# Performance work log

Hardware: AMD Instinct MI355X
Metric: run time of the kernel (lower is better)

## Reference

```python
import jax, jax.numpy as jnp
import numpy as np

N_HEADS = 4
HEAD_DIM = 64
NEG_SLOPE = 0.2
TIME_PE_DIM = 16


def time_pe(date):
    # TimePositionalEncoding: sin/cos features; 8 sin + 8 cos == pe_dim (16), no projection needed
    t = date.astype(jnp.float32) / 10000.0
    div = jnp.exp(jnp.arange(0, TIME_PE_DIM, 2, dtype=jnp.float32) * (-jnp.log(10000.0) / TIME_PE_DIM))
    arg = t[:, None] * div[None, :]  # [N, 8]
    return jnp.concatenate([jnp.sin(arg), jnp.cos(arg)], axis=-1)  # [N, 16]


def pearl_pe(x, edge_index, Wp, bp):
    # PEARL positional embedding approximated as mean-neighbor aggregation over the
    # union of all relations followed by a learned linear + tanh -> [N, 32]
    N = x.shape[0]
    src = edge_index[:, 0, :].reshape(-1)
    dst = edge_index[:, 1, :].reshape(-1)
    agg = jax.ops.segment_sum(x[src], dst, num_segments=N)
    deg = jax.ops.segment_sum(jnp.ones_like(dst, jnp.float32), dst, num_segments=N)
    agg = agg / jnp.maximum(deg, 1.0)[:, None]
    return jnp.tanh(agg @ Wp + bp)


def gatv2(x, src, dst, Wl, Wr, att, b):
    # GATv2 message passing for one edge type; dropout is identity (eval mode)
    N = x.shape[0]
    xl = (x @ Wl).reshape(N, N_HEADS, HEAD_DIM)
    xr = (x @ Wr).reshape(N, N_HEADS, HEAD_DIM)
    m = xl[src] + xr[dst]                                   # [E, H, C]
    e = jnp.sum(jax.nn.leaky_relu(m, NEG_SLOPE) * att, -1)  # [E, H]
    emax = jax.ops.segment_max(e, dst, num_segments=N)
    emax = jnp.where(jnp.isfinite(emax), emax, 0.0)
    ex = jnp.exp(e - emax[dst])
    denom = jax.ops.segment_sum(ex, dst, num_segments=N)
    alpha = ex / (denom[dst] + 1e-16)                       # segment softmax over in-edges
    out = jax.ops.segment_sum(xl[src] * alpha[..., None], dst, num_segments=N)
    return out.reshape(N, N_HEADS * HEAD_DIM) + b


def rel_agg(h_rel, W, b, a):
    # attention-weighted combination across relation outputs: h_rel [N, R, hidden]
    s = jnp.einsum('nrh,h->nr', jnp.tanh(h_rel @ W + b), a)
    w = jax.nn.softmax(s, axis=-1)
    return jnp.einsum('nr,nrh->nh', w, h_rel)


def gnn_layer(h, edge_index, Wl, Wr, att, b, aW, ab, aa):
    R = edge_index.shape[0]
    # HeteroConv aggr='sum': sum GATv2 outputs across the 5 relations
    conv_sum = gatv2(h, edge_index[0, 0], edge_index[0, 1], Wl[0], Wr[0], att[0], b[0])
    for r in range(1, R):
        conv_sum = conv_sum + gatv2(h, edge_index[r, 0], edge_index[r, 1], Wl[r], Wr[r], att[r], b[r])
    # original forward feeds conv_output['stock'] for every relation key (identical copies)
    h_rel = jnp.broadcast_to(conv_sum[:, None, :], (conv_sum.shape[0], R, conv_sum.shape[1]))
    h = rel_agg(h_rel, aW, ab, aa)
    return jax.nn.relu(h)  # dropout identity in eval


def reference(x, date_tensor, edge_index, pearl_W, pearl_b, Wl0, Wr0, att0, b0,
              Wl1, Wr1, att1, b1, aggW, aggb, agga, out_W1, out_b1, out_W2, out_b2):
    pe = pearl_pe(x, edge_index, pearl_W, pearl_b)          # [N, 32]
    tpe = time_pe(date_tensor)                              # [N, 16]
    h = jnp.concatenate([x, pe, tpe], axis=1)               # [N, 112]
    h = gnn_layer(h, edge_index, Wl0, Wr0, att0, b0, aggW[0], aggb[0], agga[0])
    h = gnn_layer(h, edge_index, Wl1, Wr1, att1, b1, aggW[1], aggb[1], agga[1])
    h = jax.nn.relu(h @ out_W1 + out_b1)
    return h @ out_W2 + out_b2                              # [N, 3]


def setup_inputs():
    key = jax.random.key(0)
    ks = jax.random.split(key, 20)
    N, E, R = 20000, 320000, 5
    IN, PE, HID = 64, 32, 256
    IN0 = IN + PE + TIME_PE_DIM  # 112

    def nrm(k, shp, sc=0.05):
        return jax.random.normal(k, shp, jnp.float32) * sc

    return {
        'x': jax.random.normal(ks[0], (N, IN), jnp.float32),
        'date_tensor': jax.random.randint(ks[1], (N,), 0, 20000, jnp.int32),
        'edge_index': jax.random.randint(ks[2], (R, 2, E), 0, N, jnp.int32),
        'pearl_W': nrm(ks[3], (IN, PE)),
        'pearl_b': jnp.zeros((PE,), jnp.float32),
        'Wl0': nrm(ks[4], (R, IN0, HID)),
        'Wr0': nrm(ks[5], (R, IN0, HID)),
        'att0': nrm(ks[6], (R, N_HEADS, HEAD_DIM)),
        'b0': jnp.zeros((R, HID), jnp.float32),
        'Wl1': nrm(ks[7], (R, HID, HID)),
        'Wr1': nrm(ks[8], (R, HID, HID)),
        'att1': nrm(ks[9], (R, N_HEADS, HEAD_DIM)),
        'b1': jnp.zeros((R, HID), jnp.float32),
        'aggW': nrm(ks[10], (2, HID, HID)),
        'aggb': jnp.zeros((2, HID), jnp.float32),
        'agga': nrm(ks[11], (2, HID)),
        'out_W1': nrm(ks[12], (HID, HID // 2)),
        'out_b1': jnp.zeros((HID // 2,), jnp.float32),
        'out_W2': nrm(ks[13], (HID // 2, 3)),
        'out_b2': jnp.zeros((3,), jnp.float32),
    }
```

## Files before the change

### kernel.cpp

```cpp
#include <hip/hip_runtime.h>
#include <math.h>

typedef __bf16 bf16x8 __attribute__((ext_vector_type(8)));
typedef __bf16 bf16x4 __attribute__((ext_vector_type(4)));
typedef float f32x4 __attribute__((ext_vector_type(4)));
typedef unsigned short u16x8 __attribute__((ext_vector_type(8)));

#define GLD16(src, dst)                                                        \
    __builtin_amdgcn_global_load_lds(                                          \
        (const __attribute__((address_space(1))) void*)(src),                  \
        (__attribute__((address_space(3))) void*)(dst), 16, 0, 0)

__device__ inline float bf2f(unsigned short u) {
    union { unsigned int i; float f; } c;
    c.i = ((unsigned int)u) << 16;
    return c.f;
}


__global__ __launch_bounds__(256) void count_kernel(const int* __restrict__ ei,
                                                    int* __restrict__ cnt, int N, int E) {
    int idx = blockIdx.x * 256 + threadIdx.x;
    if (idx >= 5 * E) return;
    int r = idx / E;
    int e = idx - r * E;
    int dst = ei[(size_t)r * 2 * E + E + e];
    atomicAdd(&cnt[r * N + dst], 1);
}

__global__ __launch_bounds__(256) void scanA_kernel(const int* __restrict__ cnt,
                                                    int* __restrict__ off,
                                                    int* __restrict__ csums, int N, int NC) {
    int r = blockIdx.y, c = blockIdx.x, t = threadIdx.x;
    int idx0 = c * 1024 + t * 4;
    int v0 = (idx0 + 0 < N) ? cnt[r * N + idx0 + 0] : 0;
    int v1 = (idx0 + 1 < N) ? cnt[r * N + idx0 + 1] : 0;
    int v2 = (idx0 + 2 < N) ? cnt[r * N + idx0 + 2] : 0;
    int v3 = (idx0 + 3 < N) ? cnt[r * N + idx0 + 3] : 0;
    int ts = v0 + v1 + v2 + v3;
    __shared__ int sd[256];
    sd[t] = ts;
    __syncthreads();
    for (int s = 1; s < 256; s <<= 1) {
        int add = (t >= s) ? sd[t - s] : 0;
        __syncthreads();
        sd[t] += add;
        __syncthreads();
    }
    int excl = sd[t] - ts;
    size_t base = (size_t)r * (N + 1);
    if (idx0 + 0 < N) off[base + idx0 + 0] = excl;
    if (idx0 + 1 < N) off[base + idx0 + 1] = excl + v0;
    if (idx0 + 2 < N) off[base + idx0 + 2] = excl + v0 + v1;
    if (idx0 + 3 < N) off[base + idx0 + 3] = excl + v0 + v1 + v2;
    if (t == 255) csums[r * NC + c] = sd[255];
}

__global__ __launch_bounds__(64) void scanB_kernel(int* __restrict__ csums,
                                                   int* __restrict__ off, int N, int NC) {
    int r = threadIdx.x;
    if (r < 5) {
        int run = 0;
        for (int c = 0; c < NC; c++) {
            int t = csums[r * NC + c];
            csums[r * NC + c] = run;
            run += t;
        }
        off[(size_t)r * (N + 1) + N] = run;
    }
}

__global__ __launch_bounds__(256) void scanC_kernel(int* __restrict__ off,
                                                    const int* __restrict__ csums,
                                                    int* __restrict__ cur,
                                                    int N, int NC) {
    int r = blockIdx.y, c = blockIdx.x, t = threadIdx.x;
    int add = csums[r * NC + c];
    int idx0 = c * 1024 + t * 4;
    size_t base = (size_t)r * (N + 1);
#pragma unroll
    for (int j = 0; j < 4; j++)
        if (idx0 + j < N) {
            int v = off[base + idx0 + j] + add;
            off[base + idx0 + j] = v;
            cur[r * N + idx0 + j] = v;
        }
}

__global__ __launch_bounds__(256) void scatter_kernel(const int* __restrict__ ei,
                                                      int* __restrict__ cur,
                                                      unsigned short* __restrict__ srcs,
                                                      int N, int E) {
    int idx = blockIdx.x * 256 + threadIdx.x;
    if (idx >= 5 * E) return;
    int r = idx / E;
    int e = idx - r * E;
    int src = ei[(size_t)r * 2 * E + e];
    int dst = ei[(size_t)r * 2 * E + E + e];
    int pos = atomicAdd(&cur[r * N + dst], 1);
    srcs[(size_t)r * E + pos] = (unsigned short)src;
}


__global__ __launch_bounds__(256) void xcvt_kernel(const float* __restrict__ x,
                                                   unsigned short* __restrict__ xb, int total) {
    int idx = (blockIdx.x * 256 + threadIdx.x) * 4;
    if (idx >= total) return;
    float4 v = *(const float4*)(x + idx);
    __bf16 b0 = (__bf16)v.x, b1 = (__bf16)v.y, b2 = (__bf16)v.z, b3 = (__bf16)v.w;
    unsigned short* p = xb + idx;
    p[0] = *(unsigned short*)&b0;
    p[1] = *(unsigned short*)&b1;
    p[2] = *(unsigned short*)&b2;
    p[3] = *(unsigned short*)&b3;
}


__global__ __launch_bounds__(256) void pearl_h0_kernel(
    const float* __restrict__ x, const unsigned short* __restrict__ xb,
    const int* __restrict__ date,
    const int* __restrict__ off, const unsigned short* __restrict__ srcs,
    const float* __restrict__ pW, const float* __restrict__ pb,
    float* __restrict__ h0, int N, int E) {
    int lane = threadIdx.x & 63;
    int wid = blockIdx.x * 4 + (threadIdx.x >> 6);
    if (wid >= N) return;
    int n = __builtin_amdgcn_readfirstlane(wid);
    int pr = lane >> 5;
    int c2 = (lane & 31) * 2;

    float a0 = 0.f, a1 = 0.f;
    int deg = 0;
    for (int r = 0; r < 5; r++) {
        int kb = off[(size_t)r * (N + 1) + n];
        int ke = off[(size_t)r * (N + 1) + n + 1];
        deg += ke - kb;
        const unsigned short* sp = srcs + (size_t)r * E;
        int k = kb;
        for (; k + 16 <= ke; k += 16) {
            unsigned int u[8];
#pragma unroll
            for (int j = 0; j < 8; j++) {
                int row = sp[k + 2 * j + pr];
                u[j] = *(const unsigned int*)(xb + (size_t)row * 64 + c2);
            }
#pragma unroll
            for (int j = 0; j < 8; j++) {
                a0 += bf2f((unsigned short)(u[j] & 0xffff));
                a1 += bf2f((unsigned short)(u[j] >> 16));
            }
        }
        for (; k + 2 <= ke; k += 2) {
            int row = sp[k + pr];
            unsigned int u = *(const unsigned int*)(xb + (size_t)row * 64 + c2);
            a0 += bf2f((unsigned short)(u & 0xffff));
            a1 += bf2f((unsigned short)(u >> 16));
        }
        if (k < ke) {
            int row = sp[k];
            unsigned int u = *(const unsigned int*)(xb + (size_t)row * 64 + c2);
            if (pr == 0) {
                a0 += bf2f((unsigned short)(u & 0xffff));
                a1 += bf2f((unsigned short)(u >> 16));
            }
        }
    }
    a0 += __shfl_xor(a0, 32, 64);
    a1 += __shfl_xor(a1, 32, 64);
    float dn = fmaxf((float)deg, 1.0f);
    float an0 = a0 / dn, an1 = a1 / dn;

    float s = (lane < 32) ? pb[lane] : 0.f;
#pragma unroll
    for (int cc = 0; cc < 64; cc++) {
        float av = __shfl((cc & 1) ? an1 : an0, cc >> 1, 64);
        if (lane < 32) s = fmaf(av, pW[cc * 32 + lane], s);
    }

    h0[(size_t)n * 112 + lane] = x[(size_t)n * 64 + lane];
    if (lane < 32) h0[(size_t)n * 112 + 64 + lane] = tanhf(s);
    if (lane < 16) {
        float t = (float)date[n] / 10000.0f;
        int i = lane & 7;
        float dv = expf((float)(2 * i) * (-0.57564627324851148f));
        float arg = t * dv;
        h0[(size_t)n * 112 + 96 + lane] = (lane < 8) ? sinf(arg) : cosf(arg);
    }
}


__global__ __launch_bounds__(256) void pack_a_kernel(
    const float* __restrict__ A, __bf16* __restrict__ Ah, __bf16* __restrict__ Al,
    int M, int K, int Mp, int KT) {
    int KG = KT * 4;
    int idx = blockIdx.x * 256 + threadIdx.x;
    if (idx >= Mp * KG) return;
    int m = idx / KG, kgg = idx - m * KG;
    int kt = kgg >> 2, kg = kgg & 3;
    int k0 = kt * 32 + kg * 8;
    int mt = m >> 4, mr = m & 15;
    size_t out = (((size_t)mt * KT + kt) * 64 + kg * 16 + mr) * 8;
    bf16x8 hv, lv;
#pragma unroll
    for (int j = 0; j < 8; j++) {
        int k = k0 + j;
        float v = (m < M && k < K) ? A[(size_t)m * K + k] : 0.f;
        __bf16 h = (__bf16)v;
        hv[j] = h;
        lv[j] = (__bf16)(v - (float)h);
    }
    *(bf16x8*)(Ah + out) = hv;
    *(bf16x8*)(Al + out) = lv;
}


__global__ __launch_bounds__(256) void pack_w_kernel(
    const float* __restrict__ Wl0, const float* __restrict__ Wr0,
    const float* __restrict__ Wl1, const float* __restrict__ Wr1,
    const float* __restrict__ W1,
    __bf16* __restrict__ Wph, __bf16* __restrict__ Wpl) {
    const int S0 = 32768, S1 = 65536;
    int t = blockIdx.y;
    const float* W;
    int K, Nc, KT;
    size_t dst;
    if (t < 5)       { W = Wl0 + (size_t)t * 112 * 256;        K = 112; Nc = 256; KT = 4; dst = (size_t)t * S0; }
    else if (t < 10) { W = Wr0 + (size_t)(t - 5) * 112 * 256;  K = 112; Nc = 256; KT = 4; dst = 163840 + (size_t)(t - 5) * S0; }
    else if (t < 15) { W = Wl1 + (size_t)(t - 10) * 256 * 256; K = 256; Nc = 256; KT = 8; dst = 327680 + (size_t)(t - 10) * S1; }
    else if (t < 20) { W = Wr1 + (size_t)(t - 15) * 256 * 256; K = 256; Nc = 256; KT = 8; dst = 655360 + (size_t)(t - 15) * S1; }
    else             { W = W1;                                  K = 256; Nc = 128; KT = 8; dst = 983040; }
    int entries = (Nc / 16) * KT * 64;
    int idx = blockIdx.x * 256 + threadIdx.x;
    if (idx >= entries) return;
    int nt = idx / (KT * 64);
    int rem = idx - nt * (KT * 64);
    int kt = rem >> 6, lane = rem & 63;
    int kg = lane >> 4, nr = lane & 15;
    bf16x8 hv, lv;
#pragma unroll
    for (int j = 0; j < 8; j++) {
        int k = kt * 32 + kg * 8 + j;
        float v = (k < K) ? W[(size_t)k * Nc + nt * 16 + nr] : 0.f;
        __bf16 h = (__bf16)v;
        hv[j] = h;
        lv[j] = (__bf16)(v - (float)h);
    }
    *(bf16x8*)(Wph + dst + (size_t)idx * 8) = hv;
    *(bf16x8*)(Wpl + dst + (size_t)idx * 8) = lv;
}


__global__ __launch_bounds__(256) void gemm_mfma(
    const __bf16* __restrict__ Ah, const __bf16* __restrict__ Al,
    const __bf16* __restrict__ WLh, const __bf16* __restrict__ WLl,
    const __bf16* __restrict__ WRh, const __bf16* __restrict__ WRl,
    size_t strideB, void* __restrict__ Cl, void* __restrict__ Cr, size_t CstrideBytes,
    int M, int Nout, int KT, const float* __restrict__ bias, int do_relu,
    int npL, int npR, int out_bf16, int NYT, int MTp, int NPANEL) {
    int p = blockIdx.x;
    int stride = 8 * NPANEL;
    int g = p / stride, rem = p % stride;
    int slot = rem % 8, panel = rem / 8;
    int bx = g * 8 + slot;
    if (bx >= MTp) return;
    int by = panel % NYT;
    int side = (panel / NYT) & 1;
    int r = panel / (NYT * 2);

    const __bf16* Bh = (side ? WRh : WLh) + (size_t)r * strideB;
    const __bf16* Bl = (side ? WRl : WLl) + (size_t)r * strideB;
    char* C = (char*)(side ? Cr : Cl) + (size_t)r * CstrideBytes;
    int np = side ? npR : npL;

    __shared__ __bf16 sAh[8 * 512], sAl[8 * 512], sBh[8 * 512], sBl[8 * 512];

    int tid = threadIdx.x, lane = tid & 63, w = tid >> 6;
    int wr = w >> 1, wc = w & 1;

    f32x4 acc[4][4] = {};

    for (int kt = 0; kt < KT; ++kt) {
        int tl = w * 2;
        size_t a0 = ((size_t)(bx * 8 + tl) * KT + kt) * 512 + lane * 8;
        size_t a1 = ((size_t)(bx * 8 + tl + 1) * KT + kt) * 512 + lane * 8;
        size_t b0 = ((size_t)(by * 8 + tl) * KT + kt) * 512 + lane * 8;
        size_t b1 = ((size_t)(by * 8 + tl + 1) * KT + kt) * 512 + lane * 8;
        GLD16(Ah + a0, sAh + tl * 512);
        GLD16(Ah + a1, sAh + (tl + 1) * 512);
        GLD16(Bh + b0, sBh + tl * 512);
        GLD16(Bh + b1, sBh + (tl + 1) * 512);
        if (np >= 2) {
            GLD16(Al + a0, sAl + tl * 512);
            GLD16(Al + a1, sAl + (tl + 1) * 512);
        }
        if (np == 3) {
            GLD16(Bl + b0, sBl + tl * 512);
            GLD16(Bl + b1, sBl + (tl + 1) * 512);
        }
        __syncthreads();

        bf16x8 ah[4], al[4], bh[4], bl[4];
#pragma unroll
        for (int i = 0; i < 4; i++) {
            ah[i] = *(const bf16x8*)(sAh + (wr * 4 + i) * 512 + lane * 8);
            bh[i] = *(const bf16x8*)(sBh + (wc * 4 + i) * 512 + lane * 8);
        }
        if (np >= 2) {
#pragma unroll
            for (int i = 0; i < 4; i++)
                al[i] = *(const bf16x8*)(sAl + (wr * 4 + i) * 512 + lane * 8);
        }
        if (np == 3) {
#pragma unroll
            for (int i = 0; i < 4; i++)
                bl[i] = *(const bf16x8*)(sBl + (wc * 4 + i) * 512 + lane * 8);
        }
#pragma unroll
        for (int i = 0; i < 4; i++)
#pragma unroll
            for (int j = 0; j < 4; j++) {
                acc[i][j] = __builtin_amdgcn_mfma_f32_16x16x32_bf16(ah[i], bh[j], acc[i][j], 0, 0, 0);
                if (np >= 2)
                    acc[i][j] = __builtin_amdgcn_mfma_f32_16x16x32_bf16(al[i], bh[j], acc[i][j], 0, 0, 0);
                if (np == 3)
                    acc[i][j] = __builtin_amdgcn_mfma_f32_16x16x32_bf16(ah[i], bl[j], acc[i][j], 0, 0, 0);
            }
        __syncthreads();
    }

    int rb = bx * 128 + wr * 64, cb = by * 128 + wc * 64;
#pragma unroll
    for (int i = 0; i < 4; i++) {
#pragma unroll
        for (int j = 0; j < 4; j++) {
            int row0 = rb + i * 16 + (lane >> 4) * 4;
            int col = cb + j * 16 + (lane & 15);
            float bv = bias ? bias[col] : 0.f;
#pragma unroll
            for (int q = 0; q < 4; q++) {
                int row = row0 + q;
                if (row < M) {
                    float v = acc[i][j][q] + bv;
                    if (do_relu) v = fmaxf(v, 0.f);
                    if (out_bf16)
                        ((__bf16*)C)[(size_t)row * Nout + col] = (__bf16)v;
                    else
                        ((float*)C)[(size_t)row * Nout + col] = v;
                }
            }
        }
    }
}


__global__ __launch_bounds__(256) void gat5_kernel(
    const unsigned short* __restrict__ xl5, const unsigned short* __restrict__ xr5,
    const float* __restrict__ att,
    const int* __restrict__ csrOff,
    const unsigned short* __restrict__ csrSrc,
    __bf16* __restrict__ Ah, __bf16* __restrict__ Al,
    const float* __restrict__ bvec,
    int N, int E) {
    int lane = threadIdx.x & 63;
    int wid = blockIdx.x * 4 + (threadIdx.x >> 6);
    if (wid >= N) return;
    int n = __builtin_amdgcn_readfirstlane(wid);
    int e = lane >> 4;
    int sub = lane & 15;
    int cb = (sub >> 2) * 64 + (sub & 3) * 16;
    int wc = cb + e * 4;

    float4 cv = {0.f, 0.f, 0.f, 0.f};
#pragma unroll
    for (int r = 0; r < 5; r++) {
        float4 b = *(const float4*)(bvec + r * 256 + wc);
        cv.x += b.x; cv.y += b.y; cv.z += b.z; cv.w += b.w;
    }

    for (int r = 0; r < 5; r++) {
        const unsigned short* xl = xl5 + (size_t)r * N * 256;
        float rv[16], av[16];
        {
            const unsigned short* xrp = xr5 + ((size_t)r * N + n) * 256 + cb;
            u16x8 q0 = *(const u16x8*)(xrp);
            u16x8 q1 = *(const u16x8*)(xrp + 8);
#pragma unroll
            for (int j = 0; j < 8; j++) { rv[j] = bf2f(q0[j]); rv[8 + j] = bf2f(q1[j]); }
#pragma unroll
            for (int j = 0; j < 16; j += 4) {
                float4 a = *(const float4*)(att + r * 256 + cb + j);
                av[j] = a.x; av[j + 1] = a.y; av[j + 2] = a.z; av[j + 3] = a.w;
            }
        }

        float m = -3.0e38f, d = 0.f;
        float A[16];
#pragma unroll
        for (int j = 0; j < 16; j++) A[j] = 0.f;

        const int* off = csrOff + (size_t)r * (N + 1);
        const unsigned short* sp = csrSrc + (size_t)r * E;
        int kb = off[n], ke = off[n + 1];
        if (kb < ke) {
            int kl = ke - 1;
            int ki = kb + e;
            int s = sp[(ki <= kl) ? ki : kl];
            float c[16];
            {
                const unsigned short* xp = xl + (size_t)s * 256 + cb;
                u16x8 q0 = *(const u16x8*)(xp);
                u16x8 q1 = *(const u16x8*)(xp + 8);
#pragma unroll
                for (int j = 0; j < 8; j++) { c[j] = bf2f(q0[j]); c[8 + j] = bf2f(q1[j]); }
            }
            for (int k = kb; k < ke; k += 4) {
                int kn = k + 4 + e;
                int sn = sp[(kn <= kl) ? kn : kl];
                const unsigned short* np_ = xl + (size_t)sn * 256 + cb;
                u16x8 n0 = *(const u16x8*)(np_);
                u16x8 n1 = *(const u16x8*)(np_ + 8);

                float p = 0.f;
#pragma unroll
                for (int j = 0; j < 16; j++) {
                    float t = c[j] + rv[j];
                    t = (t > 0.f) ? t : 0.2f * t;
                    p = fmaf(t, av[j], p);
                }
                p += __shfl_xor(p, 1, 64);
                p += __shfl_xor(p, 2, 64);
                bool valid = (k + e) < ke;
                if (!valid) p = -3.0e38f;

                if (__any(p > m)) {
                    float nm = fmaxf(m, p);
                    float sc = __expf(m - nm);
                    d *= sc;
#pragma unroll
                    for (int j = 0; j < 16; j++) A[j] *= sc;
                    m = nm;
                }
                float wg = valid ? __expf(p - m) : 0.f;
                d += wg;
#pragma unroll
                for (int j = 0; j < 16; j++) A[j] = fmaf(wg, c[j], A[j]);

#pragma unroll
                for (int j = 0; j < 8; j++) { c[j] = bf2f(n0[j]); c[8 + j] = bf2f(n1[j]); }
            }
        }

        float M = fmaxf(m, __shfl_xor(m, 16, 64));
        M = fmaxf(M, __shfl_xor(M, 32, 64));
        float sc = __expf(m - M);
        d *= sc;
        d += __shfl_xor(d, 16, 64);
        d += __shfl_xor(d, 32, 64);
#pragma unroll
        for (int j = 0; j < 16; j++) {
            A[j] *= sc;
            A[j] += __shfl_xor(A[j], 16, 64);
            A[j] += __shfl_xor(A[j], 32, 64);
        }

        float inv = 1.0f / (d + 1e-16f);
        cv.x = fmaf(A[e * 4 + 0], inv, cv.x);
        cv.y = fmaf(A[e * 4 + 1], inv, cv.y);
        cv.z = fmaf(A[e * 4 + 2], inv, cv.z);
        cv.w = fmaf(A[e * 4 + 3], inv, cv.w);
    }

    cv.x = fmaxf(cv.x, 0.f);
    cv.y = fmaxf(cv.y, 0.f);
    cv.z = fmaxf(cv.z, 0.f);
    cv.w = fmaxf(cv.w, 0.f);
    float vv[4] = {cv.x, cv.y, cv.z, cv.w};
    bf16x4 hv, lv;
#pragma unroll
    for (int j = 0; j < 4; j++) {
        __bf16 h = (__bf16)vv[j];
        hv[j] = h;
        lv[j] = (__bf16)(vv[j] - (float)h);
    }
    size_t outp = (((size_t)(n >> 4) * 8 + (wc >> 5)) * 64 + ((wc >> 3) & 3) * 16 + (n & 15)) * 8 + (wc & 7);
    *(bf16x4*)(Ah + outp) = hv;
    *(bf16x4*)(Al + outp) = lv;
}


__global__ __launch_bounds__(256) void head_kernel(const float* __restrict__ hm,
                                                   const float* __restrict__ W2,
                                                   const float* __restrict__ b2,
                                                   float* __restrict__ out, int N) {
    int lane = threadIdx.x & 63;
    int wid = blockIdx.x * 4 + (threadIdx.x >> 6);
    if (wid >= N) return;
    int n = __builtin_amdgcn_readfirstlane(wid);
    float a0 = hm[(size_t)n * 128 + lane];
    float a1 = hm[(size_t)n * 128 + 64 + lane];
    float s0 = a0 * W2[lane * 3 + 0] + a1 * W2[(64 + lane) * 3 + 0];
    float s1 = a0 * W2[lane * 3 + 1] + a1 * W2[(64 + lane) * 3 + 1];
    float s2 = a0 * W2[lane * 3 + 2] + a1 * W2[(64 + lane) * 3 + 2];
#pragma unroll
    for (int sft = 1; sft < 64; sft <<= 1) {
        s0 += __shfl_xor(s0, sft, 64);
        s1 += __shfl_xor(s1, sft, 64);
        s2 += __shfl_xor(s2, sft, 64);
    }
    if (lane == 0) {
        out[(size_t)n * 3 + 0] = s0 + b2[0];
        out[(size_t)n * 3 + 1] = s1 + b2[1];
        out[(size_t)n * 3 + 2] = s2 + b2[2];
    }
}


extern "C" void kernel_launch(void* const* d_in, const int* in_sizes, int n_in,
                              void* d_out, int out_size, void* d_ws, size_t ws_size,
                              hipStream_t stream) {
    const float* x    = (const float*)d_in[0];
    const int* date   = (const int*)d_in[1];
    const int* ei     = (const int*)d_in[2];
    const float* pW   = (const float*)d_in[3];
    const float* pb   = (const float*)d_in[4];
    const float* Wl0  = (const float*)d_in[5];
    const float* Wr0  = (const float*)d_in[6];
    const float* att0 = (const float*)d_in[7];
    const float* b0   = (const float*)d_in[8];
    const float* Wl1  = (const float*)d_in[9];
    const float* Wr1  = (const float*)d_in[10];
    const float* att1 = (const float*)d_in[11];
    const float* b1   = (const float*)d_in[12];
    const float* outW1 = (const float*)d_in[16];
    const float* outb1 = (const float*)d_in[17];
    const float* outW2 = (const float*)d_in[18];
    const float* outb2 = (const float*)d_in[19];
    float* out = (float*)d_out;

    int N = in_sizes[0] / 64;
    int E = in_sizes[2] / 10;
    int Mp = ((N + 127) / 128) * 128;
    int MT = Mp / 128;
    int MT8 = (MT + 7) / 8;
    int NC = (N + 1023) / 1024;

    char* ws = (char*)d_ws;
    size_t o = 0;
    auto alloc = [&](size_t bytes) -> char* {
        char* p = ws + o;
        o += (bytes + 255) & ~(size_t)255;
        return p;
    };
    int* cur               = (int*)alloc((size_t)5 * N * 4);
    int* csrOff            = (int*)alloc((size_t)5 * (N + 1) * 4);
    unsigned short* csrSrc = (unsigned short*)alloc((size_t)5 * E * 2);
    int* csums             = (int*)alloc((size_t)5 * NC * 4);
    unsigned short* xb16   = (unsigned short*)alloc((size_t)N * 64 * 2);
    float* h0              = (float*)alloc((size_t)N * 112 * 4);
    unsigned short* xl5    = (unsigned short*)alloc((size_t)5 * N * 256 * 2);
    unsigned short* xr5    = (unsigned short*)alloc((size_t)5 * N * 256 * 2);
    __bf16* Aph            = (__bf16*)alloc((size_t)Mp * 256 * 2);
    __bf16* Apl            = (__bf16*)alloc((size_t)Mp * 256 * 2);
    __bf16* Wph            = (__bf16*)alloc((size_t)1015808 * 2);
    __bf16* Wpl            = (__bf16*)alloc((size_t)1015808 * 2);
    float* hmid            = (float*)xl5;
    (void)ws_size;

    const size_t S0 = 32768, S1 = 65536;
    const size_t oWl0 = 0, oWr0 = 163840, oWl1 = 327680, oWr1 = 655360, oW1 = 983040;
    size_t xstride = (size_t)N * 256 * 2;

    int totE = 5 * E;

    hipMemsetAsync(cur, 0, (size_t)5 * N * 4, stream);
    count_kernel<<<(totE + 255) / 256, 256, 0, stream>>>(ei, cur, N, E);
    scanA_kernel<<<dim3(NC, 5), 256, 0, stream>>>(cur, csrOff, csums, N, NC);
    scanB_kernel<<<1, 64, 0, stream>>>(csums, csrOff, N, NC);
    scanC_kernel<<<dim3(NC, 5), 256, 0, stream>>>(csrOff, csums, cur, N, NC);
    scatter_kernel<<<(totE + 255) / 256, 256, 0, stream>>>(ei, cur, csrSrc, N, E);

    xcvt_kernel<<<(N * 64 / 4 + 255) / 256, 256, 0, stream>>>(x, xb16, N * 64);
    pearl_h0_kernel<<<(N + 3) / 4, 256, 0, stream>>>(x, xb16, date, csrOff, csrSrc, pW, pb, h0, N, E);

    pack_w_kernel<<<dim3(32, 21, 1), 256, 0, stream>>>(Wl0, Wr0, Wl1, Wr1, outW1, Wph, Wpl);

    pack_a_kernel<<<(Mp * 16 + 255) / 256, 256, 0, stream>>>(h0, Aph, Apl, N, 112, Mp, 4);
    gemm_mfma<<<MT8 * 8 * 20, 256, 0, stream>>>(
        Aph, Apl, Wph + oWl0, Wpl + oWl0, Wph + oWr0, Wpl + oWr0, S0,
        xl5, xr5, xstride, N, 256, 4, nullptr, 0, 1, 1, 1, 2, MT, 20);
    gat5_kernel<<<(N + 3) / 4, 256, 0, stream>>>(xl5, xr5, att0, csrOff, csrSrc,
                                                 Aph, Apl, b0, N, E);

    gemm_mfma<<<MT8 * 8 * 20, 256, 0, stream>>>(
        Aph, Apl, Wph + oWl1, Wpl + oWl1, Wph + oWr1, Wpl + oWr1, S1,
        xl5, xr5, xstride, N, 256, 8, nullptr, 0, 1, 1, 1, 2, MT, 20);
    gat5_kernel<<<(N + 3) / 4, 256, 0, stream>>>(xl5, xr5, att1, csrOff, csrSrc,
                                                 Aph, Apl, b1, N, E);

    gemm_mfma<<<MT8 * 8, 256, 0, stream>>>(
        Aph, Apl, Wph + oW1, Wpl + oW1, Wph + oW1, Wpl + oW1, 0,
        hmid, hmid, 0, N, 128, 8, outb1, 1, 3, 3, 0, 1, MT, 1);
    head_kernel<<<(N + 3) / 4, 256, 0, stream>>>(hmid, outW2, outb2, out, N);
}
```

Measured before the change: 749.9 us.

## Skip unused low-part bf16 writes and load two K-tiles per GEMM barrier

The low-order bf16 split of the activations and weights is now written only where a GEMM actually reads it: the final layer's input and the output-projection weights. The layer GEMMs, which run with one precision pass, no longer produce dead stores. The GEMM also moves to dynamic shared memory and, in the layer GEMMs, loads two K-tiles per synchronisation, which halves the barrier count and issues more loads in flight. The cost is a larger LDS footprint per block (32 KB), which could lower occupancy.

```diff
diff --git a/kernel.cpp b/kernel.cpp
--- a/kernel.cpp
+++ b/kernel.cpp
@@ -191,7 +191,7 @@
 
 __global__ __launch_bounds__(256) void pack_a_kernel(
     const float* __restrict__ A, __bf16* __restrict__ Ah, __bf16* __restrict__ Al,
-    int M, int K, int Mp, int KT) {
+    int M, int K, int Mp, int KT, int write_lo) {
     int KG = KT * 4;
     int idx = blockIdx.x * 256 + threadIdx.x;
     if (idx >= Mp * KG) return;
@@ -210,7 +210,7 @@
         lv[j] = (__bf16)(v - (float)h);
     }
     *(bf16x8*)(Ah + out) = hv;
-    *(bf16x8*)(Al + out) = lv;
+    if (write_lo) *(bf16x8*)(Al + out) = lv;
 }
 
 
@@ -246,7 +246,7 @@
         lv[j] = (__bf16)(v - (float)h);
     }
     *(bf16x8*)(Wph + dst + (size_t)idx * 8) = hv;
-    *(bf16x8*)(Wpl + dst + (size_t)idx * 8) = lv;
+    if (t == 20) *(bf16x8*)(Wpl + dst + (size_t)idx * 8) = lv;
 }
 
 
@@ -256,7 +256,13 @@
     const __bf16* __restrict__ WRh, const __bf16* __restrict__ WRl,
     size_t strideB, void* __restrict__ Cl, void* __restrict__ Cr, size_t CstrideBytes,
     int M, int Nout, int KT, const float* __restrict__ bias, int do_relu,
-    int npL, int npR, int out_bf16, int NYT, int MTp, int NPANEL) {
+    int npL, int npR, int out_bf16, int NYT, int MTp, int NPANEL, int kstep) {
+    extern __shared__ __bf16 smem[];
+    __bf16* sA = smem;
+    __bf16* sAl_ = smem + 4096;
+    __bf16* sB = smem + 8192;
+    __bf16* sBl_ = smem + 12288;
+
     int p = blockIdx.x;
     int stride = 8 * NPANEL;
     int g = p / stride, rem = p % stride;
@@ -272,59 +278,62 @@
     char* C = (char*)(side ? Cr : Cl) + (size_t)r * CstrideBytes;
     int np = side ? npR : npL;
 
-    __shared__ __bf16 sAh[8 * 512], sAl[8 * 512], sBh[8 * 512], sBl[8 * 512];
-
     int tid = threadIdx.x, lane = tid & 63, w = tid >> 6;
     int wr = w >> 1, wc = w & 1;
+    int tl = w * 2;
 
     f32x4 acc[4][4] = {};
 
-    for (int kt = 0; kt < KT; ++kt) {
-        int tl = w * 2;
-        size_t a0 = ((size_t)(bx * 8 + tl) * KT + kt) * 512 + lane * 8;
-        size_t a1 = ((size_t)(bx * 8 + tl + 1) * KT + kt) * 512 + lane * 8;
-        size_t b0 = ((size_t)(by * 8 + tl) * KT + kt) * 512 + lane * 8;
-        size_t b1 = ((size_t)(by * 8 + tl + 1) * KT + kt) * 512 + lane * 8;
-        GLD16(Ah + a0, sAh + tl * 512);
-        GLD16(Ah + a1, sAh + (tl + 1) * 512);
-        GLD16(Bh + b0, sBh + tl * 512);
-        GLD16(Bh + b1, sBh + (tl + 1) * 512);
-        if (np >= 2) {
-            GLD16(Al + a0, sAl + tl * 512);
-            GLD16(Al + a1, sAl + (tl + 1) * 512);
-        }
-        if (np == 3) {
-            GLD16(Bl + b0, sBl + tl * 512);
-            GLD16(Bl + b1, sBl + (tl + 1) * 512);
+    for (int kt = 0; kt < KT; kt += kstep) {
+        for (int kk = 0; kk < kstep; kk++) {
+            int ktc = kt + kk;
+            size_t a0 = ((size_t)(bx * 8 + tl) * KT + ktc) * 512 + lane * 8;
+            size_t a1 = ((size_t)(bx * 8 + tl + 1) * KT + ktc) * 512 + lane * 8;
+            size_t b0 = ((size_t)(by * 8 + tl) * KT + ktc) * 512 + lane * 8;
+            size_t b1 = ((size_t)(by * 8 + tl + 1) * KT + ktc) * 512 + lane * 8;
+            GLD16(Ah + a0, sA + kk * 4096 + tl * 512);
+            GLD16(Ah + a1, sA + kk * 4096 + (tl + 1) * 512);
+            GLD16(Bh + b0, sB + kk * 4096 + tl * 512);
+            GLD16(Bh + b1, sB + kk * 4096 + (tl + 1) * 512);
+            if (np >= 2) {
+                GLD16(Al + a0, sAl_ + tl * 512);
+                GLD16(Al + a1, sAl_ + (tl + 1) * 512);
+            }
+            if (np == 3) {
+                GLD16(Bl + b0, sBl_ + tl * 512);
+                GLD16(Bl + b1, sBl_ + (tl + 1) * 512);
+            }
         }
         __syncthreads();
 
-        bf16x8 ah[4], al[4], bh[4], bl[4];
-#pragma unroll
-        for (int i = 0; i < 4; i++) {
-            ah[i] = *(const bf16x8*)(sAh + (wr * 4 + i) * 512 + lane * 8);
-            bh[i] = *(const bf16x8*)(sBh + (wc * 4 + i) * 512 + lane * 8);
-        }
-        if (np >= 2) {
+        for (int kk = 0; kk < kstep; kk++) {
+            bf16x8 ah[4], al[4], bh[4], bl[4];
+#pragma unroll
+            for (int i = 0; i < 4; i++) {
+                ah[i] = *(const bf16x8*)(sA + kk * 4096 + (wr * 4 + i) * 512 + lane * 8);
+                bh[i] = *(const bf16x8*)(sB + kk * 4096 + (wc * 4 + i) * 512 + lane * 8);
+            }
+            if (np >= 2) {
+#pragma unroll
+                for (int i = 0; i < 4; i++)
+                    al[i] = *(const bf16x8*)(sAl_ + (wr * 4 + i) * 512 + lane * 8);
+            }
+            if (np == 3) {
+#pragma unroll
+                for (int i = 0; i < 4; i++)
+                    bl[i] = *(const bf16x8*)(sBl_ + (wc * 4 + i) * 512 + lane * 8);
+            }
 #pragma unroll
             for (int i = 0; i < 4; i++)
-                al[i] = *(const bf16x8*)(sAl + (wr * 4 + i) * 512 + lane * 8);
-        }
-        if (np == 3) {
-#pragma unroll
-            for (int i = 0; i < 4; i++)
-                bl[i] = *(const bf16x8*)(sBl + (wc * 4 + i) * 512 + lane * 8);
-        }
-#pragma unroll
-        for (int i = 0; i < 4; i++)
-#pragma unroll
-            for (int j = 0; j < 4; j++) {
-                acc[i][j] = __builtin_amdgcn_mfma_f32_16x16x32_bf16(ah[i], bh[j], acc[i][j], 0, 0, 0);
-                if (np >= 2)
-                    acc[i][j] = __builtin_amdgcn_mfma_f32_16x16x32_bf16(al[i], bh[j], acc[i][j], 0, 0, 0);
-                if (np == 3)
-                    acc[i][j] = __builtin_amdgcn_mfma_f32_16x16x32_bf16(ah[i], bl[j], acc[i][j], 0, 0, 0);
-            }
+#pragma unroll
+                for (int j = 0; j < 4; j++) {
+                    acc[i][j] = __builtin_amdgcn_mfma_f32_16x16x32_bf16(ah[i], bh[j], acc[i][j], 0, 0, 0);
+                    if (np >= 2)
+                        acc[i][j] = __builtin_amdgcn_mfma_f32_16x16x32_bf16(al[i], bh[j], acc[i][j], 0, 0, 0);
+                    if (np == 3)
+                        acc[i][j] = __builtin_amdgcn_mfma_f32_16x16x32_bf16(ah[i], bl[j], acc[i][j], 0, 0, 0);
+                }
+        }
         __syncthreads();
     }
 
@@ -360,7 +369,7 @@
     const unsigned short* __restrict__ csrSrc,
     __bf16* __restrict__ Ah, __bf16* __restrict__ Al,
     const float* __restrict__ bvec,
-    int N, int E) {
+    int N, int E, int write_lo) {
     int lane = threadIdx.x & 63;
     int wid = blockIdx.x * 4 + (threadIdx.x >> 6);
     if (wid >= N) return;
@@ -484,7 +493,7 @@
     }
     size_t outp = (((size_t)(n >> 4) * 8 + (wc >> 5)) * 64 + ((wc >> 3) & 3) * 16 + (n & 15)) * 8 + (wc & 7);
     *(bf16x4*)(Ah + outp) = hv;
-    *(bf16x4*)(Al + outp) = lv;
+    if (write_lo) *(bf16x4*)(Al + outp) = lv;
 }
 
 
@@ -571,6 +580,7 @@
     size_t xstride = (size_t)N * 256 * 2;
 
     int totE = 5 * E;
+    const size_t GEMM_LDS = 32768;
 
     hipMemsetAsync(cur, 0, (size_t)5 * N * 4, stream);
     count_kernel<<<(totE + 255) / 256, 256, 0, stream>>>(ei, cur, N, E);
@@ -584,21 +594,21 @@
 
     pack_w_kernel<<<dim3(32, 21, 1), 256, 0, stream>>>(Wl0, Wr0, Wl1, Wr1, outW1, Wph, Wpl);
 
-    pack_a_kernel<<<(Mp * 16 + 255) / 256, 256, 0, stream>>>(h0, Aph, Apl, N, 112, Mp, 4);
-    gemm_mfma<<<MT8 * 8 * 20, 256, 0, stream>>>(
+    pack_a_kernel<<<(Mp * 16 + 255) / 256, 256, 0, stream>>>(h0, Aph, Apl, N, 112, Mp, 4, 0);
+    gemm_mfma<<<MT8 * 8 * 20, 256, GEMM_LDS, stream>>>(
         Aph, Apl, Wph + oWl0, Wpl + oWl0, Wph + oWr0, Wpl + oWr0, S0,
-        xl5, xr5, xstride, N, 256, 4, nullptr, 0, 1, 1, 1, 2, MT, 20);
+        xl5, xr5, xstride, N, 256, 4, nullptr, 0, 1, 1, 1, 2, MT, 20, 2);
     gat5_kernel<<<(N + 3) / 4, 256, 0, stream>>>(xl5, xr5, att0, csrOff, csrSrc,
-                                                 Aph, Apl, b0, N, E);
-
-    gemm_mfma<<<MT8 * 8 * 20, 256, 0, stream>>>(
+                                                 Aph, Apl, b0, N, E, 0);
+
+    gemm_mfma<<<MT8 * 8 * 20, 256, GEMM_LDS, stream>>>(
         Aph, Apl, Wph + oWl1, Wpl + oWl1, Wph + oWr1, Wpl + oWr1, S1,
-        xl5, xr5, xstride, N, 256, 8, nullptr, 0, 1, 1, 1, 2, MT, 20);
+        xl5, xr5, xstride, N, 256, 8, nullptr, 0, 1, 1, 1, 2, MT, 20, 2);
     gat5_kernel<<<(N + 3) / 4, 256, 0, stream>>>(xl5, xr5, att1, csrOff, csrSrc,
-                                                 Aph, Apl, b1, N, E);
-
-    gemm_mfma<<<MT8 * 8, 256, 0, stream>>>(
+                                                 Aph, Apl, b1, N, E, 1);
+
+    gemm_mfma<<<MT8 * 8, 256, GEMM_LDS, stream>>>(
         Aph, Apl, Wph + oW1, Wpl + oW1, Wph + oW1, Wpl + oW1, 0,
-        hmid, hmid, 0, N, 128, 8, outb1, 1, 3, 3, 0, 1, MT, 1);
+        hmid, hmid, 0, N, 128, 8, outb1, 1, 3, 3, 0, 1, MT, 1, 1);
     head_kernel<<<(N + 3) / 4, 256, 0, stream>>>(hmid, outW2, outb2, out, N);
 }
```

Measured after the change: 747.7 us. No clear change (-0.3%).
